# Kernel tuning notes

Hardware: AMD Instinct MI355X
Metric: run time of the kernel (lower is better)

## Reference

```python
import jax, jax.numpy as jnp
import numpy as np

EMBED_DIM = 584
HEADS = 8
HEAD_SIZE = EMBED_DIM // HEADS  # 73
CTX = 200


def setup_inputs() -> dict:
    key = jax.random.key(0)
    ks = jax.random.split(key, 6)
    B, T = 256, 200
    x = jax.random.normal(ks[0], (B, T, EMBED_DIM), dtype=jnp.float32)
    s = 1.0 / np.sqrt(EMBED_DIM)
    # per-head q/k/v Linear(EMBED_DIM, HEAD_SIZE, bias=False) weights, stacked: [H, hs, E]
    Wq = jax.random.uniform(ks[1], (HEADS, HEAD_SIZE, EMBED_DIM), jnp.float32, -s, s)
    Wk = jax.random.uniform(ks[2], (HEADS, HEAD_SIZE, EMBED_DIM), jnp.float32, -s, s)
    Wv = jax.random.uniform(ks[3], (HEADS, HEAD_SIZE, EMBED_DIM), jnp.float32, -s, s)
    Wo = jax.random.uniform(ks[4], (EMBED_DIM, EMBED_DIM), jnp.float32, -s, s)
    bo = jax.random.uniform(ks[5], (EMBED_DIM,), jnp.float32, -s, s)
    return {"x": x, "Wq": Wq, "Wk": Wk, "Wv": Wv, "Wo": Wo, "bo": bo}


def reference(x, Wq, Wk, Wv, Wo, bo):
    B, T, C = x.shape  # C == EMBED_DIM
    # per-head projections, batched: [B, H, T, hs]
    q = jnp.einsum('bte,hfe->bhtf', x, Wq)
    k = jnp.einsum('bte,hfe->bhtf', x, Wk)
    v = jnp.einsum('bte,hfe->bhtf', x, Wv)
    # NOTE: original scales by EMBED_DIM**-0.5 (C), not head_size**-0.5
    scores = jnp.einsum('bhtf,bhsf->bhts', q, k) * (C ** -0.5)
    causal = jnp.tril(jnp.ones((T, T), dtype=bool))
    scores = jnp.where(causal, scores, -jnp.inf)
    w = jax.nn.softmax(scores, axis=-1)
    out = jnp.einsum('bhts,bhsf->bhtf', w, v)  # [B,H,T,hs]
    out = out.transpose(0, 2, 1, 3).reshape(B, T, C)  # concat heads on last dim
    return out @ Wo.T + bo
```

## Files before the change

### kernel.cpp

```cpp
#include <hip/hip_runtime.h>

typedef __bf16 bf16x8 __attribute__((ext_vector_type(8)));
typedef __bf16 bf16x4 __attribute__((ext_vector_type(4)));
typedef float f32x4 __attribute__((ext_vector_type(4)));

#define EMBED 584
#define KP 608
#define HEADS 8
#define HS 73
#define HSQ 80
#define CTX 200
#define NBATCH 256
#define MROWS 51200
#define NQKV 1752

#define PSS 232

__device__ __forceinline__ void gld_lds16(__bf16* lds, const __bf16* g) {
  __builtin_amdgcn_global_load_lds(
      (const __attribute__((address_space(1))) void*)g,
      (__attribute__((address_space(3))) void*)lds, 16, 0, 0);
}

__global__ __launch_bounds__(256) void cvt_x(const float* __restrict__ x,
                                             __bf16* __restrict__ out) {
  int i = blockIdx.x * 256 + threadIdx.x;
  int r = i / 76, slot = i - r * 76;
  int col = slot * 8;
  bf16x8 o8 = {};
  if (col < EMBED) {
    const float4* s4 = (const float4*)(x + (size_t)r * EMBED + col);
    float4 f0 = s4[0], f1 = s4[1];
    o8[0] = (__bf16)f0.x; o8[1] = (__bf16)f0.y; o8[2] = (__bf16)f0.z; o8[3] = (__bf16)f0.w;
    o8[4] = (__bf16)f1.x; o8[5] = (__bf16)f1.y; o8[6] = (__bf16)f1.z; o8[7] = (__bf16)f1.w;
  }
  *(bf16x8*)(out + (size_t)r * KP + col) = o8;
}

__global__ __launch_bounds__(256) void pack_w(const float* __restrict__ Wq,
                                              const float* __restrict__ Wk,
                                              const float* __restrict__ Wv,
                                              const float* __restrict__ Wo,
                                              __bf16* __restrict__ out) {
  int i = blockIdx.x * 256 + threadIdx.x;
  if (i >= 2336 * 76) return;
  int r = i / 76, slot = i - r * 76;
  int col = slot * 8;
  bf16x8 o8 = {};
  if (col < EMBED) {
    const float* src = r < 584  ? Wq + (size_t)r * EMBED
                     : r < 1168 ? Wk + (size_t)(r - 584) * EMBED
                     : r < 1752 ? Wv + (size_t)(r - 1168) * EMBED
                                : Wo + (size_t)(r - 1752) * EMBED;
    const float4* s4 = (const float4*)(src + col);
    float4 f0 = s4[0], f1 = s4[1];
    o8[0] = (__bf16)f0.x; o8[1] = (__bf16)f0.y; o8[2] = (__bf16)f0.z; o8[3] = (__bf16)f0.w;
    o8[4] = (__bf16)f1.x; o8[5] = (__bf16)f1.y; o8[6] = (__bf16)f1.z; o8[7] = (__bf16)f1.w;
  }
  *(bf16x8*)(out + (size_t)r * KP + col) = o8;
}

__global__ __launch_bounds__(256) void zero_pads(__bf16* __restrict__ qb,
                                                 __bf16* __restrict__ kb,
                                                 __bf16* __restrict__ vb) {
  int bh = blockIdx.x;
  bf16x8 z = {};
  __bf16* qp = qb + (size_t)bh * 16000;
  __bf16* kp = kb + (size_t)bh * 16000;
  __bf16* vp = vb + (size_t)bh * 16000;
  for (int i = threadIdx.x; i < 575; i += 256) {
    if (i < 200)      *(bf16x8*)&qp[i * 80 + 72] = z;
    else if (i < 400) *(bf16x8*)&kp[(i - 200) * 80 + 72] = z;
    else              *(bf16x8*)&vp[14600 + (i - 400) * 8] = z;
  }
}

__global__ __launch_bounds__(256) void gemm_qkv(const __bf16* __restrict__ A,
                                                const __bf16* __restrict__ Bm,
                                                __bf16* __restrict__ Q,
                                                __bf16* __restrict__ Ko,
                                                __bf16* __restrict__ V) {
  __shared__ __bf16 As[2][4096];
  __shared__ __bf16 Bs[2][4096];
  int tid = threadIdx.x;
  int id = blockIdx.x;
  int idp = (id & 7) * 700 + (id >> 3);
  int bm = idp / 14, bn = idp - bm * 14;
  int wid = tid >> 6, lane = tid & 63;
  int wm = (wid & 1) * 64, wn = (wid >> 1) * 64;
  int lr = lane & 15, lq = lane >> 4;
  const __bf16* aB = A  + (size_t)(bm * 128 + wid * 32 + (lane >> 2)) * KP + (lane & 3) * 8;
  const __bf16* bB = Bm + (size_t)(bn * 128 + wid * 32 + (lane >> 2)) * KP + (lane & 3) * 8;
  f32x4 acc[4][4] = {};
  gld_lds16(As[0] + wid * 1024,       aB);
  gld_lds16(As[0] + wid * 1024 + 512, aB + 16 * KP);
  gld_lds16(Bs[0] + wid * 1024,       bB);
  gld_lds16(Bs[0] + wid * 1024 + 512, bB + 16 * KP);
  __syncthreads();
  int cur = 0;
  for (int kt = 0; kt < 19; ++kt) {
    if (kt < 18) {
      int k0 = (kt + 1) * 32;
      gld_lds16(As[cur ^ 1] + wid * 1024,       aB + k0);
      gld_lds16(As[cur ^ 1] + wid * 1024 + 512, aB + 16 * KP + k0);
      gld_lds16(Bs[cur ^ 1] + wid * 1024,       bB + k0);
      gld_lds16(Bs[cur ^ 1] + wid * 1024 + 512, bB + 16 * KP + k0);
    }
    bf16x8 af[4], bfr[4];
#pragma unroll
    for (int i = 0; i < 4; ++i)
      af[i] = *(const bf16x8*)&As[cur][(wm + i * 16 + lr) * 32 + lq * 8];
#pragma unroll
    for (int j = 0; j < 4; ++j)
      bfr[j] = *(const bf16x8*)&Bs[cur][(wn + j * 16 + lr) * 32 + lq * 8];
#pragma unroll
    for (int i = 0; i < 4; ++i)
#pragma unroll
      for (int j = 0; j < 4; ++j)
        acc[i][j] = __builtin_amdgcn_mfma_f32_16x16x32_bf16(af[i], bfr[j], acc[i][j], 0, 0, 0);
    if (kt < 18) __syncthreads();
    cur ^= 1;
  }
  int whichj[4], ojv[4];
  __bf16* Pj[4];
  bool okj[4];
#pragma unroll
  for (int j = 0; j < 4; ++j) {
    int n = bn * 128 + wn + j * 16 + lr;
    okj[j] = (n < NQKV);
    int nn = okj[j] ? n : 0;
    int which = nn / EMBED;
    int rem = nn - which * EMBED;
    int hh = rem / HS;
    int f = rem - hh * HS;
    whichj[j] = which;
    ojv[j] = (which == 2) ? (hh * 16000 + f * 200) : (hh * 16000 + f);
    Pj[j] = (which == 0) ? Q : (which == 1) ? Ko : V;
  }
#pragma unroll
  for (int i = 0; i < 4; ++i) {
    int m0 = bm * 128 + wm + i * 16 + lq * 4;
    int bb = m0 / CTX;
    int tt = m0 - bb * CTX;
    int a_qk = bb * 128000 + tt * 80;
    int a_v  = bb * 128000 + tt;
#pragma unroll
    for (int j = 0; j < 4; ++j) {
      if (!okj[j]) continue;
      if (whichj[j] == 2) {
        bf16x4 v4;
#pragma unroll
        for (int r = 0; r < 4; ++r) v4[r] = (__bf16)acc[i][j][r];
        *(bf16x4*)&Pj[j][a_v + ojv[j]] = v4;
      } else {
        int base = a_qk + ojv[j];
#pragma unroll
        for (int r = 0; r < 4; ++r)
          Pj[j][base + r * 80] = (__bf16)acc[i][j][r];
      }
    }
  }
}

__global__ __launch_bounds__(256, 4) void attn_kernel(const __bf16* __restrict__ q,
                                                      const __bf16* __restrict__ k,
                                                      const __bf16* __restrict__ v,
                                                      __bf16* __restrict__ o) {
  __shared__ __align__(16) __bf16 Ps[4][16 * PSS];
  int tid = threadIdx.x;
  int bh = blockIdx.x;
  int b = bh >> 3, h = bh & 7;
  const __bf16* qg = q + (size_t)bh * 16000;
  const __bf16* kg = k + (size_t)bh * 16000;
  const __bf16* vg = v + (size_t)bh * 16000;

  if (h == 0) {
    bf16x8 z = {};
    for (int i = tid; i < CTX * 3; i += 256) {
      int t = i / 3, seg = i - t * 3;
      *(bf16x8*)&o[((size_t)(b * CTX + t)) * KP + EMBED + seg * 8] = z;
    }
  }

  int wid = tid >> 6, lane = tid & 63;
  int lr = lane & 15, g = lane >> 4;
  __bf16* Pw = Ps[wid];
  const float scale = 0.04138029443264672f;

  int sl[4];
  sl[0] = 12 - wid;
  sl[1] = (wid < 3) ? 6 + wid : 5;
  sl[2] = (wid < 3) ? 1 + wid : 4;
  sl[3] = (wid < 3) ? -1 : 0;

#pragma unroll
  for (int si = 0; si < 4; ++si) {
    int s = sl[si];
    if (s < 0) continue;
    int row0 = s * 16;
    bf16x8 qf[3];
    qf[0] = *(const bf16x8*)&qg[(size_t)(row0 + lr) * HSQ + g * 8];
    qf[1] = *(const bf16x8*)&qg[(size_t)(row0 + lr) * HSQ + 32 + g * 8];
    qf[2] = (g < 2) ? *(const bf16x8*)&qg[(size_t)(row0 + lr) * HSQ + 64 + g * 8]
                    : bf16x8{};
    float sc[13][4];
#pragma unroll
    for (int nt = 0; nt < 13; ++nt) {
      if (nt > s) continue;
      f32x4 acc = {};
#pragma unroll
      for (int kc = 0; kc < 3; ++kc) {
        bf16x8 kf = *(const bf16x8*)&kg[(size_t)(nt * 16 + lr) * HSQ + kc * 32 + g * 8];
        acc = __builtin_amdgcn_mfma_f32_16x16x32_bf16(qf[kc], kf, acc, 0, 0, 0);
      }
#pragma unroll
      for (int r = 0; r < 4; ++r) {
        float val = acc[r] * scale;
        if (nt == s && lr > g * 4 + r) val = -1e30f;
        if (nt * 16 + lr >= CTX) val = -1e30f;
        sc[nt][r] = val;
      }
    }
    float mr[4], rs[4];
#pragma unroll
    for (int r = 0; r < 4; ++r) {
      float m = -1e30f;
#pragma unroll
      for (int nt = 0; nt < 13; ++nt)
        if (nt <= s) m = fmaxf(m, sc[nt][r]);
      mr[r] = m;
    }
#pragma unroll
    for (int off = 8; off; off >>= 1)
#pragma unroll
      for (int r = 0; r < 4; ++r)
        mr[r] = fmaxf(mr[r], __shfl_xor(mr[r], off, 64));
#pragma unroll
    for (int r = 0; r < 4; ++r) {
      float ssum = 0.f;
#pragma unroll
      for (int nt = 0; nt < 13; ++nt) {
        if (nt > s) continue;
        sc[nt][r] = __expf(sc[nt][r] - mr[r]);
        ssum += sc[nt][r];
      }
      rs[r] = ssum;
    }
#pragma unroll
    for (int off = 8; off; off >>= 1)
#pragma unroll
      for (int r = 0; r < 4; ++r) rs[r] += __shfl_xor(rs[r], off, 64);
#pragma unroll
    for (int nt = 0; nt < 13; ++nt) {
      if (nt > s) continue;
#pragma unroll
      for (int r = 0; r < 4; ++r)
        Pw[(g * 4 + r) * PSS + nt * 16 + lr] = (__bf16)sc[nt][r];
    }
    if ((s & 1) == 0) {
#pragma unroll
      for (int r = 0; r < 4; ++r)
        Pw[(g * 4 + r) * PSS + (s + 1) * 16 + lr] = (__bf16)0.f;
    }
    f32x4 ov[5];
#pragma unroll
    for (int nt = 0; nt < 5; ++nt) ov[nt] = f32x4{0.f, 0.f, 0.f, 0.f};
#pragma unroll
    for (int kc = 0; kc < 7; ++kc) {
      if (kc > s / 2) continue;
      bf16x8 pf = *(const bf16x8*)&Pw[lr * PSS + kc * 32 + g * 8];
#pragma unroll
      for (int nt = 0; nt < 5; ++nt) {
        bf16x8 vf = *(const bf16x8*)&vg[(size_t)(nt * 16 + lr) * CTX + kc * 32 + g * 8];
        ov[nt] = __builtin_amdgcn_mfma_f32_16x16x32_bf16(pf, vf, ov[nt], 0, 0, 0);
      }
    }
    float inv[4];
#pragma unroll
    for (int r = 0; r < 4; ++r) inv[r] = 1.0f / rs[r];
#pragma unroll
    for (int nt = 0; nt < 5; ++nt) {
      int f = nt * 16 + lr;
      if (f < HS) {
#pragma unroll
        for (int r = 0; r < 4; ++r) {
          int t = row0 + g * 4 + r;
          if (t < CTX)
            o[((size_t)(b * CTX + t)) * KP + h * HS + f] =
                (__bf16)(ov[nt][r] * inv[r]);
        }
      }
    }
  }
}

__global__ __launch_bounds__(256) void gemm_out(const __bf16* __restrict__ A,
                                                const __bf16* __restrict__ Bm,
                                                const float* __restrict__ bias,
                                                float* __restrict__ C) {
  constexpr int N = EMBED;
  __shared__ __bf16 As[2][4096];
  __shared__ __bf16 Bs[2][4096];
  int tid = threadIdx.x;
  int id = blockIdx.x;
  int idp = (id & 7) * 250 + (id >> 3);
  int bm = idp / 5, bn = idp - bm * 5;
  int wid = tid >> 6, lane = tid & 63;
  int wm = (wid & 1) * 64, wn = (wid >> 1) * 64;
  int lr = lane & 15, lq = lane >> 4;
  const __bf16* aB = A  + (size_t)(bm * 128 + wid * 32 + (lane >> 2)) * KP + (lane & 3) * 8;
  const __bf16* bB = Bm + (size_t)(bn * 128 + wid * 32 + (lane >> 2)) * KP + (lane & 3) * 8;
  f32x4 acc[4][4] = {};
  gld_lds16(As[0] + wid * 1024,       aB);
  gld_lds16(As[0] + wid * 1024 + 512, aB + 16 * KP);
  gld_lds16(Bs[0] + wid * 1024,       bB);
  gld_lds16(Bs[0] + wid * 1024 + 512, bB + 16 * KP);
  __syncthreads();
  int cur = 0;
  for (int kt = 0; kt < 19; ++kt) {
    if (kt < 18) {
      int k0 = (kt + 1) * 32;
      gld_lds16(As[cur ^ 1] + wid * 1024,       aB + k0);
      gld_lds16(As[cur ^ 1] + wid * 1024 + 512, aB + 16 * KP + k0);
      gld_lds16(Bs[cur ^ 1] + wid * 1024,       bB + k0);
      gld_lds16(Bs[cur ^ 1] + wid * 1024 + 512, bB + 16 * KP + k0);
    }
    bf16x8 af[4], bfr[4];
#pragma unroll
    for (int i = 0; i < 4; ++i)
      af[i] = *(const bf16x8*)&As[cur][(wm + i * 16 + lr) * 32 + lq * 8];
#pragma unroll
    for (int j = 0; j < 4; ++j)
      bfr[j] = *(const bf16x8*)&Bs[cur][(wn + j * 16 + lr) * 32 + lq * 8];
#pragma unroll
    for (int i = 0; i < 4; ++i)
#pragma unroll
      for (int j = 0; j < 4; ++j)
        acc[i][j] = __builtin_amdgcn_mfma_f32_16x16x32_bf16(af[i], bfr[j], acc[i][j], 0, 0, 0);
    if (kt < 18) __syncthreads();
    cur ^= 1;
  }
#pragma unroll
  for (int i = 0; i < 4; ++i) {
    int m = bm * 128 + wm + i * 16 + lq * 4;
#pragma unroll
    for (int j = 0; j < 4; ++j) {
      int n = bn * 128 + wn + j * 16 + lr;
      if (n < N) {
        float bval = bias[n];
#pragma unroll
        for (int r = 0; r < 4; ++r)
          C[(size_t)(m + r) * N + n] = acc[i][j][r] + bval;
      }
    }
  }
}

extern "C" void kernel_launch(void* const* d_in, const int* in_sizes, int n_in,
                              void* d_out, int out_size, void* d_ws, size_t ws_size,
                              hipStream_t stream) {
  const float* x  = (const float*)d_in[0];
  const float* Wq = (const float*)d_in[1];
  const float* Wk = (const float*)d_in[2];
  const float* Wv = (const float*)d_in[3];
  const float* Wo = (const float*)d_in[4];
  const float* bo = (const float*)d_in[5];
  float* out = (float*)d_out;

  __bf16* wcat = (__bf16*)d_ws;
  __bf16* vb   = wcat + 1420288ULL;
  __bf16* qb   = vb + 32768000ULL;
  __bf16* kb   = qb + 32768000ULL;
  __bf16* xb   = kb + 32768000ULL;
  __bf16* ab   = xb;

  cvt_x<<<15200, 256, 0, stream>>>(x, xb);
  pack_w<<<694, 256, 0, stream>>>(Wq, Wk, Wv, Wo, wcat);
  zero_pads<<<2048, 256, 0, stream>>>(qb, kb, vb);
  gemm_qkv<<<5600, 256, 0, stream>>>(xb, wcat, qb, kb, vb);
  attn_kernel<<<2048, 256, 0, stream>>>(qb, kb, vb, ab);
  gemm_out<<<2000, 256, 0, stream>>>(ab, wcat + 1752ULL * KP, bo, out);
}
```

Before: 684.0 us.

## Triple-buffer LDS loads in QKV and output GEMMs with one barrier per step

```diff
diff --git a/kernel.cpp b/kernel.cpp
--- a/kernel.cpp
+++ b/kernel.cpp
@@ -80,8 +80,8 @@
                                                 __bf16* __restrict__ Q,
                                                 __bf16* __restrict__ Ko,
                                                 __bf16* __restrict__ V) {
-  __shared__ __bf16 As[2][4096];
-  __shared__ __bf16 Bs[2][4096];
+  __shared__ __bf16 As[3][4096];
+  __shared__ __bf16 Bs[3][4096];
   int tid = threadIdx.x;
   int id = blockIdx.x;
   int idp = (id & 7) * 700 + (id >> 3);
@@ -92,35 +92,42 @@
   const __bf16* aB = A  + (size_t)(bm * 128 + wid * 32 + (lane >> 2)) * KP + (lane & 3) * 8;
   const __bf16* bB = Bm + (size_t)(bn * 128 + wid * 32 + (lane >> 2)) * KP + (lane & 3) * 8;
   f32x4 acc[4][4] = {};
-  gld_lds16(As[0] + wid * 1024,       aB);
-  gld_lds16(As[0] + wid * 1024 + 512, aB + 16 * KP);
-  gld_lds16(Bs[0] + wid * 1024,       bB);
-  gld_lds16(Bs[0] + wid * 1024 + 512, bB + 16 * KP);
-  __syncthreads();
-  int cur = 0;
+
+#define STAGE_QKV(buf, kt)                                        \
+  do {                                                            \
+    int k0_ = (kt) * 32;                                          \
+    gld_lds16(As[buf] + wid * 1024,       aB + k0_);              \
+    gld_lds16(As[buf] + wid * 1024 + 512, aB + 16 * KP + k0_);    \
+    gld_lds16(Bs[buf] + wid * 1024,       bB + k0_);              \
+    gld_lds16(Bs[buf] + wid * 1024 + 512, bB + 16 * KP + k0_);    \
+  } while (0)
+
+  STAGE_QKV(0, 0);
+  STAGE_QKV(1, 1);
+#pragma unroll
   for (int kt = 0; kt < 19; ++kt) {
-    if (kt < 18) {
-      int k0 = (kt + 1) * 32;
-      gld_lds16(As[cur ^ 1] + wid * 1024,       aB + k0);
-      gld_lds16(As[cur ^ 1] + wid * 1024 + 512, aB + 16 * KP + k0);
-      gld_lds16(Bs[cur ^ 1] + wid * 1024,       bB + k0);
-      gld_lds16(Bs[cur ^ 1] + wid * 1024 + 512, bB + 16 * KP + k0);
-    }
+    if (kt < 18) asm volatile("s_waitcnt vmcnt(4)" ::: "memory");
+    else         asm volatile("s_waitcnt vmcnt(0)" ::: "memory");
+    __builtin_amdgcn_s_barrier();
+    if (kt + 2 < 19) STAGE_QKV((kt + 2) % 3, kt + 2);
+    const __bf16* Ac = As[kt % 3];
+    const __bf16* Bc = Bs[kt % 3];
     bf16x8 af[4], bfr[4];
 #pragma unroll
     for (int i = 0; i < 4; ++i)
-      af[i] = *(const bf16x8*)&As[cur][(wm + i * 16 + lr) * 32 + lq * 8];
+      af[i] = *(const bf16x8*)&Ac[(wm + i * 16 + lr) * 32 + lq * 8];
 #pragma unroll
     for (int j = 0; j < 4; ++j)
-      bfr[j] = *(const bf16x8*)&Bs[cur][(wn + j * 16 + lr) * 32 + lq * 8];
+      bfr[j] = *(const bf16x8*)&Bc[(wn + j * 16 + lr) * 32 + lq * 8];
+    __builtin_amdgcn_s_setprio(1);
 #pragma unroll
     for (int i = 0; i < 4; ++i)
 #pragma unroll
       for (int j = 0; j < 4; ++j)
         acc[i][j] = __builtin_amdgcn_mfma_f32_16x16x32_bf16(af[i], bfr[j], acc[i][j], 0, 0, 0);
-    if (kt < 18) __syncthreads();
-    cur ^= 1;
-  }
+    __builtin_amdgcn_s_setprio(0);
+  }
+#undef STAGE_QKV
   int whichj[4], ojv[4];
   __bf16* Pj[4];
   bool okj[4];
@@ -299,8 +306,8 @@
                                                 const float* __restrict__ bias,
                                                 float* __restrict__ C) {
   constexpr int N = EMBED;
-  __shared__ __bf16 As[2][4096];
-  __shared__ __bf16 Bs[2][4096];
+  __shared__ __bf16 As[3][4096];
+  __shared__ __bf16 Bs[3][4096];
   int tid = threadIdx.x;
   int id = blockIdx.x;
   int idp = (id & 7) * 250 + (id >> 3);
@@ -311,35 +318,42 @@
   const __bf16* aB = A  + (size_t)(bm * 128 + wid * 32 + (lane >> 2)) * KP + (lane & 3) * 8;
   const __bf16* bB = Bm + (size_t)(bn * 128 + wid * 32 + (lane >> 2)) * KP + (lane & 3) * 8;
   f32x4 acc[4][4] = {};
-  gld_lds16(As[0] + wid * 1024,       aB);
-  gld_lds16(As[0] + wid * 1024 + 512, aB + 16 * KP);
-  gld_lds16(Bs[0] + wid * 1024,       bB);
-  gld_lds16(Bs[0] + wid * 1024 + 512, bB + 16 * KP);
-  __syncthreads();
-  int cur = 0;
+
+#define STAGE_OUT(buf, kt)                                        \
+  do {                                                            \
+    int k0_ = (kt) * 32;                                          \
+    gld_lds16(As[buf] + wid * 1024,       aB + k0_);              \
+    gld_lds16(As[buf] + wid * 1024 + 512, aB + 16 * KP + k0_);    \
+    gld_lds16(Bs[buf] + wid * 1024,       bB + k0_);              \
+    gld_lds16(Bs[buf] + wid * 1024 + 512, bB + 16 * KP + k0_);    \
+  } while (0)
+
+  STAGE_OUT(0, 0);
+  STAGE_OUT(1, 1);
+#pragma unroll
   for (int kt = 0; kt < 19; ++kt) {
-    if (kt < 18) {
-      int k0 = (kt + 1) * 32;
-      gld_lds16(As[cur ^ 1] + wid * 1024,       aB + k0);
-      gld_lds16(As[cur ^ 1] + wid * 1024 + 512, aB + 16 * KP + k0);
-      gld_lds16(Bs[cur ^ 1] + wid * 1024,       bB + k0);
-      gld_lds16(Bs[cur ^ 1] + wid * 1024 + 512, bB + 16 * KP + k0);
-    }
+    if (kt < 18) asm volatile("s_waitcnt vmcnt(4)" ::: "memory");
+    else         asm volatile("s_waitcnt vmcnt(0)" ::: "memory");
+    __builtin_amdgcn_s_barrier();
+    if (kt + 2 < 19) STAGE_OUT((kt + 2) % 3, kt + 2);
+    const __bf16* Ac = As[kt % 3];
+    const __bf16* Bc = Bs[kt % 3];
     bf16x8 af[4], bfr[4];
 #pragma unroll
     for (int i = 0; i < 4; ++i)
-      af[i] = *(const bf16x8*)&As[cur][(wm + i * 16 + lr) * 32 + lq * 8];
+      af[i] = *(const bf16x8*)&Ac[(wm + i * 16 + lr) * 32 + lq * 8];
 #pragma unroll
     for (int j = 0; j < 4; ++j)
-      bfr[j] = *(const bf16x8*)&Bs[cur][(wn + j * 16 + lr) * 32 + lq * 8];
+      bfr[j] = *(const bf16x8*)&Bc[(wn + j * 16 + lr) * 32 + lq * 8];
+    __builtin_amdgcn_s_setprio(1);
 #pragma unroll
     for (int i = 0; i < 4; ++i)
 #pragma unroll
       for (int j = 0; j < 4; ++j)
         acc[i][j] = __builtin_amdgcn_mfma_f32_16x16x32_bf16(af[i], bfr[j], acc[i][j], 0, 0, 0);
-    if (kt < 18) __syncthreads();
-    cur ^= 1;
-  }
+    __builtin_amdgcn_s_setprio(0);
+  }
+#undef STAGE_OUT
 #pragma unroll
   for (int i = 0; i < 4; ++i) {
     int m = bm * 128 + wm + i * 16 + lq * 4;
```

Result: faster. 654.1 us (-4.4%).
